# Kernel tuning notes

Measured on AMD Instinct MI355X. Metric: run time of the kernel, lower is better.

## Reference

```python
import jax, jax.numpy as jnp
import numpy as np

DM, NE, ES, ESZ = 1024, 16, 4, 64  # dm, nexperts, expertsets, expertsize (dff = NE*ES*ESZ = 4096)
BATCH, SEQ = 8, 2048


def setup_inputs() -> dict:
    key = jax.random.key(0)
    k = jax.random.split(key, 5)
    scale = 0.02
    return {
        "x": jax.random.normal(k[0], (BATCH, SEQ, DM), dtype=jnp.float32),
        "controller": jax.random.normal(k[1], (DM, NE, ES), dtype=jnp.float32) * scale,
        "f1": jax.random.normal(k[2], (DM, NE, ES, ESZ), dtype=jnp.float32) * scale,
        "f2": jax.random.normal(k[3], (NE, ES, ESZ, DM), dtype=jnp.float32) * scale,
        "bias": jax.random.normal(k[4], (NE, ES, ESZ), dtype=jnp.float32) * scale,
    }


def reference(x, controller, f1, f2, bias):
    ne = controller.shape[1]
    d = x.shape[-1]
    # group tokens: [..., (b t), d] -> [..., b, t, d] with t = nexperts
    grouped = x.reshape(x.shape[:-2] + (-1, ne, d))
    # controller logits per token/expert/expertset: [..., b, t, e, s]
    logits = jnp.einsum('...btd,des->...btes', grouped, controller)
    # deterministic tiebreaker over the token-within-group axis t
    tie = jnp.linspace(0.0, 1e-6, ne, dtype=logits.dtype).reshape(ne, 1, 1)
    logits = logits + tie
    # hard top-1 permutation: for each (e, s) pick the argmax token t (one-hot over t)
    perm = (logits == jnp.max(logits, axis=-3, keepdims=True)).astype(x.dtype)
    # dispatch: select the chosen token's activations per (e, s): [..., b, e, s, d]
    sel = jnp.einsum('...btd,...btes->...besd', grouped, perm)
    # expert FFN up-projection + bias + relu: [..., b, e, s, f]
    inner = jax.nn.relu(jnp.einsum('...besd,desf->...besf', sel, f1) + bias)
    # expert FFN down-projection: [..., b, e, s, d]
    inter = jnp.einsum('...besf,esfd->...besd', inner, f2)
    # un-permute back to token positions: [..., b, t, d]
    out = jnp.einsum('...besd,...btes->...btd', inter, perm)
    return out.reshape(x.shape)
```

## Files before the change

kernel.cpp:

```cpp
#include <hip/hip_runtime.h>

#define DM   1024
#define NES  64
#define ESZ  64
#define NG   1024
#define TOK  16

typedef __bf16 bf16;
typedef __bf16 bf16x4 __attribute__((ext_vector_type(4)));
typedef __bf16 bf16x8 __attribute__((ext_vector_type(8)));
typedef float  f32x4  __attribute__((ext_vector_type(4)));

__global__ __launch_bounds__(256) void k0_transpose(const float* __restrict__ f1,
                                                    const float* __restrict__ f2,
                                                    bf16* __restrict__ f1p,
                                                    bf16* __restrict__ f2t) {
    __shared__ float tile[64 * 65];
    const int es = blockIdx.y, d0 = blockIdx.x * 64, tid = threadIdx.x;
    #pragma unroll
    for (int i = 0; i < 4; ++i) {
        int idx = i * 256 + tid; int r = idx >> 4, c4 = (idx & 15) * 4;
        float4 v = *(const float4*)(f1 + (size_t)(d0 + r) * 4096 + es * 64 + c4);
        tile[r * 65 + c4] = v.x; tile[r * 65 + c4 + 1] = v.y;
        tile[r * 65 + c4 + 2] = v.z; tile[r * 65 + c4 + 3] = v.w;
    }
    __syncthreads();
    #pragma unroll
    for (int i = 0; i < 2; ++i) {
        int idx = i * 256 + tid; int f = idx >> 3, dl0 = (idx & 7) * 8;
        bf16x8 o;
        #pragma unroll
        for (int j = 0; j < 8; ++j) o[j] = (bf16)tile[(dl0 + j) * 65 + f];
        *(bf16x8*)(f1p + (size_t)es * 65536 + f * 1024 + d0 + dl0) = o;
    }
    __syncthreads();
    #pragma unroll
    for (int i = 0; i < 4; ++i) {
        int idx = i * 256 + tid; int r = idx >> 4, c4 = (idx & 15) * 4;
        float4 v = *(const float4*)(f2 + (size_t)es * 65536 + r * 1024 + d0 + c4);
        tile[r * 65 + c4] = v.x; tile[r * 65 + c4 + 1] = v.y;
        tile[r * 65 + c4 + 2] = v.z; tile[r * 65 + c4 + 3] = v.w;
    }
    __syncthreads();
    #pragma unroll
    for (int i = 0; i < 2; ++i) {
        int idx = i * 256 + tid; int dl = idx >> 3, f0 = (idx & 7) * 8;
        bf16x8 o;
        #pragma unroll
        for (int j = 0; j < 8; ++j) o[j] = (bf16)tile[(f0 + j) * 65 + dl];
        *(bf16x8*)(f2t + (size_t)es * 65536 + (size_t)(d0 + dl) * 64 + f0) = o;
    }
}

__global__ __launch_bounds__(256) void k1_logits(const float* __restrict__ x,
                                                 const float* __restrict__ ctrl,
                                                 int* __restrict__ sel,
                                                 unsigned* __restrict__ selp) {
    __shared__ __align__(16) float xs[TOK * 132];
    __shared__ float sl[TOK * NES];
    __shared__ int   st[NES];
    const int bg  = blockIdx.x;
    const int tid = threadIdx.x;
    const int es  = tid & 63;
    const int tq  = tid >> 6;
    const float* xg = x + (size_t)bg * (TOK * DM);
    const float* cp = ctrl + es;
    float acc[4] = {0.f, 0.f, 0.f, 0.f};
    for (int d0 = 0; d0 < DM; d0 += 128) {
        __syncthreads();
        #pragma unroll
        for (int c = 0; c < 2; ++c) {
            int idx = tid + c * 256;
            int tr  = idx >> 5;
            int c4  = (idx & 31) * 4;
            float4 v = *(const float4*)(xg + tr * DM + d0 + c4);
            *(float4*)(xs + tr * 132 + c4) = v;
        }
        __syncthreads();
        #pragma unroll 2
        for (int dl4 = 0; dl4 < 128; dl4 += 4) {
            float4 v0 = *(const float4*)(xs + (tq * 4 + 0) * 132 + dl4);
            float4 v1 = *(const float4*)(xs + (tq * 4 + 1) * 132 + dl4);
            float4 v2 = *(const float4*)(xs + (tq * 4 + 2) * 132 + dl4);
            float4 v3 = *(const float4*)(xs + (tq * 4 + 3) * 132 + dl4);
            float c0 = cp[(size_t)(d0 + dl4 + 0) * 64];
            float c1 = cp[(size_t)(d0 + dl4 + 1) * 64];
            float c2 = cp[(size_t)(d0 + dl4 + 2) * 64];
            float c3 = cp[(size_t)(d0 + dl4 + 3) * 64];
            acc[0] += v0.x * c0; acc[1] += v1.x * c0;
            acc[2] += v2.x * c0; acc[3] += v3.x * c0;
            acc[0] += v0.y * c1; acc[1] += v1.y * c1;
            acc[2] += v2.y * c1; acc[3] += v3.y * c1;
            acc[0] += v0.z * c2; acc[1] += v1.z * c2;
            acc[2] += v2.z * c2; acc[3] += v3.z * c2;
            acc[0] += v0.w * c3; acc[1] += v1.w * c3;
            acc[2] += v2.w * c3; acc[3] += v3.w * c3;
        }
    }
    #pragma unroll
    for (int i = 0; i < 4; ++i) {
        int t = tq * 4 + i;
        sl[t * NES + es] = acc[i] + (float)t * (1e-6f / 15.f);
    }
    __syncthreads();
    if (tid < NES) {
        float best = -1e30f; int bi = 0;
        #pragma unroll
        for (int t = 0; t < TOK; ++t) {
            float v = sl[t * NES + tid];
            if (v >= best) { best = v; bi = t; }
        }
        sel[bg * NES + tid] = bi;
        st[tid] = bi;
    }
    __syncthreads();
    if (tid < 8) {
        unsigned p = 0;
        #pragma unroll
        for (int k = 0; k < 8; ++k) p |= (unsigned)st[tid * 8 + k] << (4 * k);
        selp[bg * 8 + tid] = p;
    }
}

__global__ __launch_bounds__(256) void k2_ffn1(const float* __restrict__ x,
                                               const bf16* __restrict__ f1p,
                                               const float* __restrict__ bias,
                                               const int* __restrict__ sel,
                                               bf16* __restrict__ inner) {
    __shared__ int  sel_s[128];
    __shared__ __align__(16) bf16 As[128 * 40];
    __shared__ __align__(16) bf16 Bs[64 * 40];
    const int es  = blockIdx.y;
    const int g0  = blockIdx.x * 128;
    const int tid = threadIdx.x;
    if (tid < 128) sel_s[tid] = sel[(g0 + tid) * 64 + es];
    __syncthreads();

    const int w = tid >> 6, l = tid & 63, quad = l >> 4, lr = l & 15;
    int tokrow[4];
    #pragma unroll
    for (int p = 0; p < 4; ++p) {
        int grow = p * 32 + (tid >> 3);
        tokrow[p] = (g0 + grow) * 16 + sel_s[grow];
    }
    const int c4 = (tid & 7) * 4;
    const int bf = tid >> 2, bd = (tid & 3) * 8;
    const bf16* f1es = f1p + (size_t)es * (DM * ESZ);

    f32x4 acc[2][4];
    #pragma unroll
    for (int mt = 0; mt < 2; ++mt)
        #pragma unroll
        for (int nt = 0; nt < 4; ++nt)
            acc[mt][nt] = (f32x4){0.f, 0.f, 0.f, 0.f};

    for (int k0 = 0; k0 < DM; k0 += 32) {
        #pragma unroll
        for (int p = 0; p < 4; ++p) {
            int grow = p * 32 + (tid >> 3);
            float4 v = *(const float4*)(x + (size_t)tokrow[p] * DM + k0 + c4);
            bf16x4 ob = {(bf16)v.x, (bf16)v.y, (bf16)v.z, (bf16)v.w};
            *(bf16x4*)(As + grow * 40 + c4) = ob;
        }
        {
            bf16x8 v = *(const bf16x8*)(f1es + bf * 1024 + k0 + bd);
            *(bf16x8*)(Bs + bf * 40 + bd) = v;
        }
        __syncthreads();
        bf16x8 av[2], bv[4];
        #pragma unroll
        for (int mt = 0; mt < 2; ++mt)
            av[mt] = *(const bf16x8*)(As + (w * 32 + mt * 16 + lr) * 40 + quad * 8);
        #pragma unroll
        for (int nt = 0; nt < 4; ++nt)
            bv[nt] = *(const bf16x8*)(Bs + (nt * 16 + lr) * 40 + quad * 8);
        #pragma unroll
        for (int mt = 0; mt < 2; ++mt)
            #pragma unroll
            for (int nt = 0; nt < 4; ++nt)
                acc[mt][nt] = __builtin_amdgcn_mfma_f32_16x16x32_bf16(
                    av[mt], bv[nt], acc[mt][nt], 0, 0, 0);
        __syncthreads();
    }
    bf16* innes = inner + (size_t)es * (NG * ESZ);
    #pragma unroll
    for (int mt = 0; mt < 2; ++mt)
        #pragma unroll
        for (int nt = 0; nt < 4; ++nt) {
            int f = nt * 16 + lr;
            float b = bias[es * 64 + f];
            #pragma unroll
            for (int r = 0; r < 4; ++r) {
                int grow = w * 32 + mt * 16 + quad * 4 + r;
                float v = acc[mt][nt][r] + b;
                v = v > 0.f ? v : 0.f;
                innes[(size_t)(g0 + grow) * 64 + f] = (bf16)v;
            }
        }
}

__global__ __launch_bounds__(256) void k3_ffn2(const bf16* __restrict__ inner,
                                               const bf16* __restrict__ f2t,
                                               const unsigned* __restrict__ selp,
                                               float* __restrict__ out) {
    __shared__ float accs[512 * 32];
    const int d0  = blockIdx.x * 32;
    const int g0  = blockIdx.y * 32;
    const int tid = threadIdx.x;
    const int w = tid >> 6, l = tid & 63, quad = l >> 4, lr = l & 15;
    const int mh = w >> 1, nh = w & 1;

    unsigned sp[4][8];
    #pragma unroll
    for (int r = 0; r < 4; ++r) {
        int gl = mh * 16 + quad * 4 + r;
        uint4 a = *(const uint4*)(selp + (size_t)(g0 + gl) * 8);
        uint4 b = *(const uint4*)(selp + (size_t)(g0 + gl) * 8 + 4);
        sp[r][0] = a.x; sp[r][1] = a.y; sp[r][2] = a.z; sp[r][3] = a.w;
        sp[r][4] = b.x; sp[r][5] = b.y; sp[r][6] = b.z; sp[r][7] = b.w;
    }
    #pragma unroll
    for (int i = 0; i < 16; ++i)
        ((float4*)accs)[i * 256 + tid] = (float4){0.f, 0.f, 0.f, 0.f};

    const bf16* pa = inner + (size_t)(g0 + mh * 16 + lr) * 64 + quad * 8;
    const bf16* pb = f2t   + (size_t)(d0 + nh * 16 + lr) * 64 + quad * 8;

    bf16x8 A[4][2], B[4][2];
    #pragma unroll
    for (int s = 0; s < 2; ++s) {
        const bf16* qa = pa + (size_t)s * 65536;
        const bf16* qb = pb + (size_t)s * 65536;
        A[s][0] = *(const bf16x8*)(qa);
        A[s][1] = *(const bf16x8*)(qa + 32);
        B[s][0] = *(const bf16x8*)(qb);
        B[s][1] = *(const bf16x8*)(qb + 32);
    }
    __syncthreads();

    #pragma unroll
    for (int es = 0; es < 64; ++es) {
        const int lp = (es + 2) & 3;
        const bf16* qa = pa + (size_t)(es + 2) * 65536;
        const bf16* qb = pb + (size_t)(es + 2) * 65536;
        A[lp][0] = *(const bf16x8*)(qa);
        A[lp][1] = *(const bf16x8*)(qa + 32);
        B[lp][0] = *(const bf16x8*)(qb);
        B[lp][1] = *(const bf16x8*)(qb + 32);

        const int s = es & 3;
        f32x4 z = {0.f, 0.f, 0.f, 0.f};
        z = __builtin_amdgcn_mfma_f32_16x16x32_bf16(A[s][0], B[s][0], z, 0, 0, 0);
        z = __builtin_amdgcn_mfma_f32_16x16x32_bf16(A[s][1], B[s][1], z, 0, 0, 0);

        const int dw = es >> 3, sh = (es & 7) * 4;
        #pragma unroll
        for (int r = 0; r < 4; ++r) {
            int t    = (sp[r][dw] >> sh) & 15;
            int gl   = mh * 16 + quad * 4 + r;
            int scol = (nh * 16 + lr) ^ ((t & 7) << 2);
            accs[(gl * 16 + t) * 32 + scol] += z[r];
        }
    }
    __syncthreads();
    #pragma unroll
    for (int i = 0; i < 16; ++i) {
        int fi = i * 256 + tid;
        int row = fi >> 3, q = fi & 7;
        int scol4 = (q * 4) ^ ((row & 7) << 2);
        float4 v = *(float4*)(accs + row * 32 + scol4);
        *(float4*)(out + (size_t)(g0 * 16 + row) * DM + d0 + q * 4) = v;
    }
}

extern "C" void kernel_launch(void* const* d_in, const int* in_sizes, int n_in,
                              void* d_out, int out_size, void* d_ws, size_t ws_size,
                              hipStream_t stream) {
    const float* x    = (const float*)d_in[0];
    const float* ctrl = (const float*)d_in[1];
    const float* f1   = (const float*)d_in[2];
    const float* f2   = (const float*)d_in[3];
    const float* bias = (const float*)d_in[4];
    float* out = (float*)d_out;

    char* ws = (char*)d_ws;
    bf16*     f1p   = (bf16*)(ws);
    bf16*     f2t   = (bf16*)(ws + 8388608);
    bf16*     inner = (bf16*)(ws + 16777216);
    int*      sel   = (int*)(ws + 25165824);
    unsigned* selp  = (unsigned*)(ws + 25427968);

    hipLaunchKernelGGL(k0_transpose, dim3(16, 64), dim3(256), 0, stream, f1, f2, f1p, f2t);
    hipLaunchKernelGGL(k1_logits,    dim3(1024),   dim3(256), 0, stream, x, ctrl, sel, selp);
    hipLaunchKernelGGL(k2_ffn1,      dim3(8, 64),  dim3(256), 0, stream, x, f1p, bias, sel, inner);
    hipLaunchKernelGGL(k3_ffn2,      dim3(32, 32), dim3(256), 0, stream, inner, f2t, selp, out);
}
```

Before: 353.0 us.

## Stage FFN2 operand tiles through LDS with async global-to-LDS double buffering

Replaces the per-thread register prefetch of inner and f2t fragments in the down-projection kernel with direct global-to-LDS loads into double-buffered swizzled shared tiles, synchronised by explicit vmcnt waits and barriers per expert set. Each tile is now loaded once per block and shared across waves instead of redundantly fetched by each wave. Output stores become nontemporal. It adds two barriers per iteration and depends on hand-written waitcnt counts being correct.

Result: faster. 306.1 us (-13.3%).

```diff
diff --git a/kernel.cpp b/kernel.cpp
--- a/kernel.cpp
+++ b/kernel.cpp
@@ -10,6 +10,12 @@
 typedef __bf16 bf16x4 __attribute__((ext_vector_type(4)));
 typedef __bf16 bf16x8 __attribute__((ext_vector_type(8)));
 typedef float  f32x4  __attribute__((ext_vector_type(4)));
+
+__device__ __forceinline__ void gld_lds16(const bf16* g, bf16* s) {
+    __builtin_amdgcn_global_load_lds(
+        (const __attribute__((address_space(1))) void*)g,
+        (__attribute__((address_space(3))) void*)s, 16, 0, 0);
+}
 
 __global__ __launch_bounds__(256) void k0_transpose(const float* __restrict__ f1,
                                                     const float* __restrict__ f2,
@@ -204,6 +210,8 @@
                                                const unsigned* __restrict__ selp,
                                                float* __restrict__ out) {
     __shared__ float accs[512 * 32];
+    __shared__ __align__(16) bf16 As[2][32 * 64];
+    __shared__ __align__(16) bf16 Bs[2][32 * 64];
     const int d0  = blockIdx.x * 32;
     const int g0  = blockIdx.y * 32;
     const int tid = threadIdx.x;
@@ -219,39 +227,51 @@
         sp[r][0] = a.x; sp[r][1] = a.y; sp[r][2] = a.z; sp[r][3] = a.w;
         sp[r][4] = b.x; sp[r][5] = b.y; sp[r][6] = b.z; sp[r][7] = b.w;
     }
+
+    const int srow = tid >> 3;
+    const int scb  = ((tid & 7) * 16) ^ ((srow & 7) << 4);
+    const bf16* srcA = inner + (size_t)(g0 + srow) * 64 + (scb >> 1);
+    const bf16* srcB = f2t   + (size_t)(d0 + srow) * 64 + (scb >> 1);
+    bf16* dA0 = &As[0][w * 512]; bf16* dA1 = &As[1][w * 512];
+    bf16* dB0 = &Bs[0][w * 512]; bf16* dB1 = &Bs[1][w * 512];
+
     #pragma unroll
     for (int i = 0; i < 16; ++i)
-        ((float4*)accs)[i * 256 + tid] = (float4){0.f, 0.f, 0.f, 0.f};
-
-    const bf16* pa = inner + (size_t)(g0 + mh * 16 + lr) * 64 + quad * 8;
-    const bf16* pb = f2t   + (size_t)(d0 + nh * 16 + lr) * 64 + quad * 8;
-
-    bf16x8 A[4][2], B[4][2];
-    #pragma unroll
-    for (int s = 0; s < 2; ++s) {
-        const bf16* qa = pa + (size_t)s * 65536;
-        const bf16* qb = pb + (size_t)s * 65536;
-        A[s][0] = *(const bf16x8*)(qa);
-        A[s][1] = *(const bf16x8*)(qa + 32);
-        B[s][0] = *(const bf16x8*)(qb);
-        B[s][1] = *(const bf16x8*)(qb + 32);
-    }
-    __syncthreads();
+        ((f32x4*)accs)[i * 256 + tid] = (f32x4){0.f, 0.f, 0.f, 0.f};
+
+    gld_lds16(srcA, dA0);
+    gld_lds16(srcB, dB0);
+    __syncthreads();
+
+    const int rowA = mh * 16 + lr, rowB = nh * 16 + lr;
+    const int offA0 = rowA * 128 + ((quad * 16)      ^ ((rowA & 7) << 4));
+    const int offA1 = rowA * 128 + ((quad * 16 + 64) ^ ((rowA & 7) << 4));
+    const int offB0 = rowB * 128 + ((quad * 16)      ^ ((rowB & 7) << 4));
+    const int offB1 = rowB * 128 + ((quad * 16 + 64) ^ ((rowB & 7) << 4));
 
     #pragma unroll
     for (int es = 0; es < 64; ++es) {
-        const int lp = (es + 2) & 3;
-        const bf16* qa = pa + (size_t)(es + 2) * 65536;
-        const bf16* qb = pb + (size_t)(es + 2) * 65536;
-        A[lp][0] = *(const bf16x8*)(qa);
-        A[lp][1] = *(const bf16x8*)(qa + 32);
-        B[lp][0] = *(const bf16x8*)(qb);
-        B[lp][1] = *(const bf16x8*)(qb + 32);
-
-        const int s = es & 3;
+        const int cur = es & 1;
+        if (es < 63) {
+            if (cur == 0) { gld_lds16(srcA + (size_t)(es + 1) * 65536, dA1);
+                            gld_lds16(srcB + (size_t)(es + 1) * 65536, dB1); }
+            else          { gld_lds16(srcA + (size_t)(es + 1) * 65536, dA0);
+                            gld_lds16(srcB + (size_t)(es + 1) * 65536, dB0); }
+            asm volatile("s_waitcnt vmcnt(2)" ::: "memory");
+        } else {
+            asm volatile("s_waitcnt vmcnt(0)" ::: "memory");
+        }
+        asm volatile("s_barrier" ::: "memory");
+
+        const char* a = (const char*)As[cur];
+        const char* b = (const char*)Bs[cur];
+        bf16x8 a0 = *(const bf16x8*)(a + offA0);
+        bf16x8 a1 = *(const bf16x8*)(a + offA1);
+        bf16x8 b0 = *(const bf16x8*)(b + offB0);
+        bf16x8 b1 = *(const bf16x8*)(b + offB1);
         f32x4 z = {0.f, 0.f, 0.f, 0.f};
-        z = __builtin_amdgcn_mfma_f32_16x16x32_bf16(A[s][0], B[s][0], z, 0, 0, 0);
-        z = __builtin_amdgcn_mfma_f32_16x16x32_bf16(A[s][1], B[s][1], z, 0, 0, 0);
+        z = __builtin_amdgcn_mfma_f32_16x16x32_bf16(a0, b0, z, 0, 0, 0);
+        z = __builtin_amdgcn_mfma_f32_16x16x32_bf16(a1, b1, z, 0, 0, 0);
 
         const int dw = es >> 3, sh = (es & 7) * 4;
         #pragma unroll
@@ -261,6 +281,7 @@
             int scol = (nh * 16 + lr) ^ ((t & 7) << 2);
             accs[(gl * 16 + t) * 32 + scol] += z[r];
         }
+        asm volatile("s_barrier" ::: "memory");
     }
     __syncthreads();
     #pragma unroll
@@ -268,8 +289,8 @@
         int fi = i * 256 + tid;
         int row = fi >> 3, q = fi & 7;
         int scol4 = (q * 4) ^ ((row & 7) << 2);
-        float4 v = *(float4*)(accs + row * 32 + scol4);
-        *(float4*)(out + (size_t)(g0 * 16 + row) * DM + d0 + q * 4) = v;
+        f32x4 v = *(f32x4*)(accs + row * 32 + scol4);
+        __builtin_nontemporal_store(v, (f32x4*)(out + (size_t)(g0 * 16 + row) * DM + d0 + q * 4));
     }
 }
 
```
